# Optimization experiments

Hardware: AMD Instinct MI355X
Metric: run time of the kernel (lower is better)

Reference implementation:

```python
import jax, jax.numpy as jnp
import numpy as np

N_NODES = 100000
N_EDGES = 1600000
IN_DIM, HID_DIM, OUT_DIM = 64, 64, 16


def setup_inputs() -> dict:
    key = jax.random.key(0)
    k1, k2, k3, k4 = jax.random.split(key, 4)
    x = jax.random.normal(k1, (N_NODES, IN_DIM), dtype=jnp.float32)
    edge_index = jax.random.randint(k2, (2, N_EDGES), 0, N_NODES, dtype=jnp.int64)
    W1 = jax.random.normal(k3, (IN_DIM, HID_DIM), dtype=jnp.float32) * (1.0 / np.sqrt(IN_DIM))
    b1 = jnp.zeros((HID_DIM,), dtype=jnp.float32)
    W2 = jax.random.normal(k4, (HID_DIM, OUT_DIM), dtype=jnp.float32) * (1.0 / np.sqrt(HID_DIM))
    b2 = jnp.zeros((OUT_DIM,), dtype=jnp.float32)
    return {"x": x, "edge_index": edge_index, "W1": W1, "b1": b1, "W2": W2, "b2": b2}


def gcn_conv(x, src, dst, W, b, num_nodes):
    """GCNConv: h = D^{-1/2} (A+I) D^{-1/2} (x W) + b, edge-list form with self-loops already appended."""
    # symmetric degree normalization (degree counted at destination, incl. self-loops)
    deg = jax.ops.segment_sum(jnp.ones_like(dst, dtype=x.dtype), dst, num_segments=num_nodes)
    dinv = jnp.where(deg > 0, jax.lax.rsqrt(deg), 0.0)
    norm = dinv[src] * dinv[dst]                      # [E+N]
    h = x @ W                                         # [N, H] project first (fewer flops on edges)
    msg = h[src] * norm[:, None]                      # gather + scale, [E+N, H]
    out = jax.ops.segment_sum(msg, dst, num_segments=num_nodes)  # scatter-add
    return out + b


def reference(x, edge_index, W1, b1, W2, b2):
    num_nodes = x.shape[0]
    loop = jnp.arange(num_nodes, dtype=edge_index.dtype)
    src = jnp.concatenate([edge_index[0], loop])      # add self-loops once, reuse for both layers
    dst = jnp.concatenate([edge_index[1], loop])
    h = gcn_conv(x, src, dst, W1, b1, num_nodes)
    h = jax.nn.relu(h)
    # F.dropout(training=self.training): eval mode -> identity
    out = gcn_conv(h, src, dst, W2, b2, num_nodes)
    return out
```

## Files before the change

kernel.cpp:

```cpp
#include <hip/hip_runtime.h>

constexpr int N_NODES = 100000;
constexpr int F1 = 64;
constexpr int F2 = 16;
constexpr int SH = 7;
constexpr int NPB = 128;
constexpr int NBINS = (N_NODES + NPB - 1) / NPB;
constexpr int CAPB = 2560;
constexpr int TILE = 4096;
constexpr int GSTRIDE = 16;

static __device__ __forceinline__ unsigned short f2bf(float f) {
    unsigned int u = __float_as_uint(f);
    unsigned int r = (u + 0x7fffu + ((u >> 16) & 1u)) >> 16;
    return (unsigned short)r;
}
static __device__ __forceinline__ float bf2f(unsigned short b) {
    return __uint_as_float(((unsigned int)b) << 16);
}

__global__ __launch_bounds__(512) void k_bin(const int* __restrict__ src,
                                             const int* __restrict__ dst, int E,
                                             unsigned int* __restrict__ gcnt,
                                             unsigned int* __restrict__ entries) {
    __shared__ unsigned int cnt[NBINS];
    __shared__ unsigned int cur[NBINS];
    int tid = threadIdx.x;
    int base = blockIdx.x * TILE;
    int end = min(base + TILE, E);
    for (int i = tid; i < NBINS; i += 512) cnt[i] = 0;
    __syncthreads();
    for (int e = base + tid; e < end; e += 512) atomicAdd(&cnt[dst[e] >> SH], 1u);
    __syncthreads();
    for (int i = tid; i < NBINS; i += 512) {
        unsigned int c = cnt[i];
        cur[i] = (unsigned int)i * CAPB + (c ? atomicAdd(&gcnt[i * GSTRIDE], c) : 0u);
    }
    __syncthreads();
    for (int e = base + tid; e < end; e += 512) {
        int d = dst[e];
        int s = src[e];
        int bb = d >> SH;
        unsigned int p = atomicAdd(&cur[bb], 1u);
        if (p - (unsigned int)bb * CAPB < CAPB)
            entries[p] = (unsigned int)s | ((unsigned int)(d & (NPB - 1)) << 17);
    }
}

__global__ __launch_bounds__(512) void k_xw1(const float* __restrict__ x,
                                             const float* __restrict__ W,
                                             const unsigned int* __restrict__ gcnt,
                                             const unsigned int* __restrict__ entries,
                                             float* __restrict__ dinv,
                                             unsigned short* __restrict__ hs) {
    constexpr int XS = 68;
    __shared__ float Ws[64 * 64];
    __shared__ float xs[128 * XS];
    __shared__ unsigned int ncnt[NPB];
    __shared__ float dinvs[NPB];
    int tid = threadIdx.x;
    int b = blockIdx.x;
    int r0 = b * NPB;
    for (int i = tid; i < 1024; i += 512) {
        int k = i >> 4, c4 = (i & 15) << 2;
        *(float4*)&Ws[k * 64 + c4] = *(const float4*)&W[k * 64 + c4];
    }
    for (int i = tid; i < 2048; i += 512) {
        int rr = i >> 4, c4 = (i & 15) << 2;
        int r = r0 + rr;
        float4 v = make_float4(0.f, 0.f, 0.f, 0.f);
        if (r < N_NODES) v = *(const float4*)&x[(size_t)r * 64 + c4];
        *(float4*)&xs[rr * XS + c4] = v;
    }
    if (tid < NPB) ncnt[tid] = 0;
    __syncthreads();
    unsigned int cntE = gcnt[b * GSTRIDE]; if (cntE > CAPB) cntE = CAPB;
    unsigned int ebase = (unsigned int)b * CAPB;
    for (unsigned int e = tid; e < cntE; e += 512)
        atomicAdd(&ncnt[entries[ebase + e] >> 17], 1u);
    __syncthreads();
    if (tid < NPB) {
        int node = r0 + tid;
        float dv = rsqrtf((float)(ncnt[tid] + 1u));
        dinvs[tid] = dv;
        if (node < N_NODES) dinv[node] = dv;
    }
    __syncthreads();
    int tx = tid & 15, ty = tid >> 4;
    int c0 = tx << 2, rb = ty << 2;
    float acc[4][4] = {};
#pragma unroll 8
    for (int k = 0; k < 64; ++k) {
        float4 w = *(float4*)&Ws[k * 64 + c0];
        float x0 = xs[(rb + 0) * XS + k];
        float x1 = xs[(rb + 1) * XS + k];
        float x2 = xs[(rb + 2) * XS + k];
        float x3 = xs[(rb + 3) * XS + k];
        acc[0][0] += x0 * w.x; acc[0][1] += x0 * w.y; acc[0][2] += x0 * w.z; acc[0][3] += x0 * w.w;
        acc[1][0] += x1 * w.x; acc[1][1] += x1 * w.y; acc[1][2] += x1 * w.z; acc[1][3] += x1 * w.w;
        acc[2][0] += x2 * w.x; acc[2][1] += x2 * w.y; acc[2][2] += x2 * w.z; acc[2][3] += x2 * w.w;
        acc[3][0] += x3 * w.x; acc[3][1] += x3 * w.y; acc[3][2] += x3 * w.z; acc[3][3] += x3 * w.w;
    }
#pragma unroll
    for (int i = 0; i < 4; ++i) {
        int r = r0 + rb + i;
        if (r >= N_NODES) break;
        float dv = dinvs[rb + i];
        ushort4 p;
        p.x = f2bf(acc[i][0] * dv);
        p.y = f2bf(acc[i][1] * dv);
        p.z = f2bf(acc[i][2] * dv);
        p.w = f2bf(acc[i][3] * dv);
        *(ushort4*)&hs[(size_t)r * 64 + c0] = p;
    }
}

__global__ __launch_bounds__(1024) void k_agg1f(const unsigned int* __restrict__ gcnt,
                                                unsigned int* __restrict__ entries,
                                                unsigned int* __restrict__ noffg,
                                                const unsigned short* __restrict__ hs,
                                                const float* __restrict__ dinv,
                                                unsigned short* __restrict__ out1) {
    __shared__ unsigned int ncnt[NPB];
    __shared__ unsigned int noff[NPB + 1];
    __shared__ unsigned int cur[NPB];
    __shared__ unsigned int sl[CAPB];
    int tid = threadIdx.x;
    int b = blockIdx.x;
    unsigned int cntE = gcnt[b * GSTRIDE]; if (cntE > CAPB) cntE = CAPB;
    unsigned int base = (unsigned int)b * CAPB;
    if (tid < NPB) ncnt[tid] = 0;
    __syncthreads();
    for (unsigned int e = tid; e < cntE; e += 1024)
        atomicAdd(&ncnt[entries[base + e] >> 17], 1u);
    __syncthreads();
    if (tid < NPB) cur[tid] = ncnt[tid];
    __syncthreads();
    for (int ofs = 1; ofs < NPB; ofs <<= 1) {
        unsigned int v = (tid < NPB && tid >= ofs) ? cur[tid - ofs] : 0u;
        __syncthreads();
        if (tid < NPB) cur[tid] += v;
        __syncthreads();
    }
    if (tid < NPB) noff[tid + 1] = cur[tid];
    if (tid == 0) noff[0] = 0;
    __syncthreads();
    if (tid < NPB) cur[tid] = noff[tid];
    __syncthreads();
    for (unsigned int e = tid; e < cntE; e += 1024) {
        unsigned int v = entries[base + e];
        unsigned int p = atomicAdd(&cur[v >> 17], 1u);
        sl[p] = v & 0x1FFFFu;
    }
    __syncthreads();
    for (unsigned int e = tid; e < cntE; e += 1024) entries[base + e] = sl[e];
    if (tid <= NPB) noffg[b * (NPB + 1) + tid] = noff[tid];
    int wid = tid >> 6, k = tid & 63;
    for (int n = wid; n < NPB; n += 16) {
        int node = b * NPB + n;
        if (node >= N_NODES) break;
        unsigned int j = noff[n], jend = noff[n + 1];
        float acc = bf2f(hs[(size_t)node * 64 + k]);
        for (; j + 8 <= jend; j += 8) {
            unsigned int s0 = sl[j], s1 = sl[j + 1], s2 = sl[j + 2], s3 = sl[j + 3];
            unsigned int s4 = sl[j + 4], s5 = sl[j + 5], s6 = sl[j + 6], s7 = sl[j + 7];
            float a0 = bf2f(hs[(size_t)s0 * 64 + k]);
            float a1 = bf2f(hs[(size_t)s1 * 64 + k]);
            float a2 = bf2f(hs[(size_t)s2 * 64 + k]);
            float a3 = bf2f(hs[(size_t)s3 * 64 + k]);
            float a4 = bf2f(hs[(size_t)s4 * 64 + k]);
            float a5 = bf2f(hs[(size_t)s5 * 64 + k]);
            float a6 = bf2f(hs[(size_t)s6 * 64 + k]);
            float a7 = bf2f(hs[(size_t)s7 * 64 + k]);
            acc += ((a0 + a1) + (a2 + a3)) + ((a4 + a5) + (a6 + a7));
        }
        for (; j + 4 <= jend; j += 4) {
            unsigned int s0 = sl[j], s1 = sl[j + 1], s2 = sl[j + 2], s3 = sl[j + 3];
            float a0 = bf2f(hs[(size_t)s0 * 64 + k]);
            float a1 = bf2f(hs[(size_t)s1 * 64 + k]);
            float a2 = bf2f(hs[(size_t)s2 * 64 + k]);
            float a3 = bf2f(hs[(size_t)s3 * 64 + k]);
            acc += (a0 + a1) + (a2 + a3);
        }
        for (; j < jend; ++j) acc += bf2f(hs[(size_t)sl[j] * 64 + k]);
        out1[(size_t)node * 64 + k] = f2bf(acc * dinv[node]);
    }
}

__global__ __launch_bounds__(256) void k_xw2(const unsigned short* __restrict__ out1,
                                             const float* __restrict__ b1,
                                             const float* __restrict__ W2,
                                             const float* __restrict__ dinv,
                                             unsigned short* __restrict__ h2s) {
    constexpr int RS = 66;
    __shared__ float Ws[64 * 16];
    __shared__ float rs[128 * RS];
    __shared__ float b1s[64];
    int tid = threadIdx.x;
    int r0 = blockIdx.x * 128;
    if (tid < 64) b1s[tid] = b1[tid];
    for (int i = tid; i < 256; i += 256)
        *(float4*)&Ws[i * 4] = *(const float4*)&W2[i * 4];
    __syncthreads();
    for (int i = tid; i < 2048; i += 256) {
        int rr = i >> 4, c4 = (i & 15) << 2;
        int r = r0 + rr;
        float v0 = 0.f, v1 = 0.f, v2 = 0.f, v3 = 0.f;
        if (r < N_NODES) {
            ushort4 u = *(const ushort4*)&out1[(size_t)r * 64 + c4];
            v0 = fmaxf(bf2f(u.x) + b1s[c4 + 0], 0.f);
            v1 = fmaxf(bf2f(u.y) + b1s[c4 + 1], 0.f);
            v2 = fmaxf(bf2f(u.z) + b1s[c4 + 2], 0.f);
            v3 = fmaxf(bf2f(u.w) + b1s[c4 + 3], 0.f);
        }
        float* pp = &rs[rr * RS + c4];
        pp[0] = v0; pp[1] = v1; pp[2] = v2; pp[3] = v3;
    }
    __syncthreads();
    int tx = tid & 3, ty = tid >> 2;
    int c0 = tx << 2, rb = ty << 1;
    float acc[2][4] = {};
#pragma unroll 8
    for (int k = 0; k < 64; ++k) {
        float4 w = *(float4*)&Ws[k * 16 + c0];
        float x0 = rs[(rb + 0) * RS + k];
        float x1 = rs[(rb + 1) * RS + k];
        acc[0][0] += x0 * w.x; acc[0][1] += x0 * w.y; acc[0][2] += x0 * w.z; acc[0][3] += x0 * w.w;
        acc[1][0] += x1 * w.x; acc[1][1] += x1 * w.y; acc[1][2] += x1 * w.z; acc[1][3] += x1 * w.w;
    }
#pragma unroll
    for (int i = 0; i < 2; ++i) {
        int r = r0 + rb + i;
        if (r >= N_NODES) break;
        float dv = dinv[r];
        ushort4 p;
        p.x = f2bf(acc[i][0] * dv);
        p.y = f2bf(acc[i][1] * dv);
        p.z = f2bf(acc[i][2] * dv);
        p.w = f2bf(acc[i][3] * dv);
        *(ushort4*)&h2s[(size_t)r * 16 + c0] = p;
    }
}

__global__ __launch_bounds__(1024) void k_agg2f(const unsigned int* __restrict__ gcnt,
                                                const unsigned int* __restrict__ sorted,
                                                const unsigned int* __restrict__ noffg,
                                                const unsigned short* __restrict__ h2s,
                                                const float* __restrict__ dinv,
                                                const float* __restrict__ b2,
                                                float* __restrict__ out) {
    __shared__ unsigned int noff[NPB + 1];
    __shared__ unsigned int sl[CAPB];
    int tid = threadIdx.x;
    int b = blockIdx.x;
    unsigned int cntE = gcnt[b * GSTRIDE]; if (cntE > CAPB) cntE = CAPB;
    unsigned int base = (unsigned int)b * CAPB;
    if (tid <= NPB) noff[tid] = noffg[b * (NPB + 1) + tid];
    for (unsigned int e = tid; e < cntE; e += 1024) sl[e] = sorted[base + e];
    __syncthreads();
    int wid = tid >> 6, lane = tid & 63;
    int k = lane & 15, esub = lane >> 4;
    for (int n = wid; n < NPB; n += 16) {
        int node = b * NPB + n;
        if (node >= N_NODES) break;
        unsigned int j0 = noff[n], jend = noff[n + 1];
        float acc = 0.0f;
        unsigned int j = j0 + esub;
        for (; j + 4 < jend; j += 8) {
            float a = bf2f(h2s[(size_t)sl[j] * 16 + k]);
            float c = bf2f(h2s[(size_t)sl[j + 4] * 16 + k]);
            acc += a + c;
        }
        if (j < jend) acc += bf2f(h2s[(size_t)sl[j] * 16 + k]);
        acc += __shfl_xor(acc, 16);
        acc += __shfl_xor(acc, 32);
        if (lane < 16)
            out[(size_t)node * 16 + k] = (acc + bf2f(h2s[(size_t)node * 16 + k])) * dinv[node] + b2[k];
    }
}

static inline size_t align256(size_t x) { return (x + 255) & ~size_t(255); }

extern "C" void kernel_launch(void* const* d_in, const int* in_sizes, int n_in,
                              void* d_out, int out_size, void* d_ws, size_t ws_size,
                              hipStream_t stream) {
    const float* x  = (const float*)d_in[0];
    const int* edge = (const int*)d_in[1];
    const float* W1 = (const float*)d_in[2];
    const float* b1 = (const float*)d_in[3];
    const float* W2 = (const float*)d_in[4];
    const float* b2 = (const float*)d_in[5];
    float* out = (float*)d_out;

    const int E = in_sizes[1] / 2;
    const int* src = edge;
    const int* dst = edge + E;

    char* ws = (char*)d_ws;
    size_t o = 0;
    unsigned int* gcnt    = (unsigned int*)(ws + o); o += align256((size_t)NBINS * GSTRIDE * 4);
    float* dinv           = (float*)(ws + o);        o += align256((size_t)N_NODES * 4);
    unsigned int* entries = (unsigned int*)(ws + o); o += align256((size_t)NBINS * CAPB * 4);
    unsigned int* noffg   = (unsigned int*)(ws + o); o += align256((size_t)NBINS * (NPB + 1) * 4);
    unsigned short* hs    = (unsigned short*)(ws + o); o += align256((size_t)N_NODES * F1 * 2);
    unsigned short* out1  = (unsigned short*)(ws + o); o += align256((size_t)N_NODES * F1 * 2);
    unsigned short* h2s   = (unsigned short*)(ws + o); o += align256((size_t)N_NODES * F2 * 2);

    hipMemsetAsync(gcnt, 0, (size_t)NBINS * GSTRIDE * 4, stream);

    k_bin<<<(E + TILE - 1) / TILE, 512, 0, stream>>>(src, dst, E, gcnt, entries);

    k_xw1<<<NBINS, 512, 0, stream>>>(x, W1, gcnt, entries, dinv, hs);
    k_agg1f<<<NBINS, 1024, 0, stream>>>(gcnt, entries, noffg, hs, dinv, out1);

    k_xw2<<<(N_NODES + 127) / 128, 256, 0, stream>>>(out1, b1, W2, dinv, h2s);
    k_agg2f<<<NBINS, 1024, 0, stream>>>(gcnt, entries, noffg, h2s, dinv, b2, out);
}
```

Baseline: 144.4 us.

## Split layer-1 aggregation across two blocks per bin by feature half

```diff
diff --git a/kernel.cpp b/kernel.cpp
--- a/kernel.cpp
+++ b/kernel.cpp
@@ -116,7 +116,8 @@
 }
 
 __global__ __launch_bounds__(1024) void k_agg1f(const unsigned int* __restrict__ gcnt,
-                                                unsigned int* __restrict__ entries,
+                                                const unsigned int* __restrict__ entries,
+                                                unsigned int* __restrict__ sorted,
                                                 unsigned int* __restrict__ noffg,
                                                 const unsigned short* __restrict__ hs,
                                                 const float* __restrict__ dinv,
@@ -126,7 +127,10 @@
     __shared__ unsigned int cur[NPB];
     __shared__ unsigned int sl[CAPB];
     int tid = threadIdx.x;
-    int b = blockIdx.x;
+    int blk = blockIdx.x;
+    int half = (blk & 7) >= 4;
+    int b = ((blk >> 3) << 2) + (blk & 3);
+    if (b >= NBINS) return;
     unsigned int cntE = gcnt[b * GSTRIDE]; if (cntE > CAPB) cntE = CAPB;
     unsigned int base = (unsigned int)b * CAPB;
     if (tid < NPB) ncnt[tid] = 0;
@@ -153,37 +157,30 @@
         sl[p] = v & 0x1FFFFu;
     }
     __syncthreads();
-    for (unsigned int e = tid; e < cntE; e += 1024) entries[base + e] = sl[e];
-    if (tid <= NPB) noffg[b * (NPB + 1) + tid] = noff[tid];
-    int wid = tid >> 6, k = tid & 63;
+    if (half == 0) {
+        for (unsigned int e = tid; e < cntE; e += 1024) sorted[base + e] = sl[e];
+        if (tid <= NPB) noffg[b * (NPB + 1) + tid] = noff[tid];
+    }
+    int wid = tid >> 6, lane = tid & 63;
+    int grp = lane >> 5;
+    int c = half * 32 + (lane & 31);
     for (int n = wid; n < NPB; n += 16) {
         int node = b * NPB + n;
         if (node >= N_NODES) break;
-        unsigned int j = noff[n], jend = noff[n + 1];
-        float acc = bf2f(hs[(size_t)node * 64 + k]);
-        for (; j + 8 <= jend; j += 8) {
-            unsigned int s0 = sl[j], s1 = sl[j + 1], s2 = sl[j + 2], s3 = sl[j + 3];
-            unsigned int s4 = sl[j + 4], s5 = sl[j + 5], s6 = sl[j + 6], s7 = sl[j + 7];
-            float a0 = bf2f(hs[(size_t)s0 * 64 + k]);
-            float a1 = bf2f(hs[(size_t)s1 * 64 + k]);
-            float a2 = bf2f(hs[(size_t)s2 * 64 + k]);
-            float a3 = bf2f(hs[(size_t)s3 * 64 + k]);
-            float a4 = bf2f(hs[(size_t)s4 * 64 + k]);
-            float a5 = bf2f(hs[(size_t)s5 * 64 + k]);
-            float a6 = bf2f(hs[(size_t)s6 * 64 + k]);
-            float a7 = bf2f(hs[(size_t)s7 * 64 + k]);
-            acc += ((a0 + a1) + (a2 + a3)) + ((a4 + a5) + (a6 + a7));
-        }
-        for (; j + 4 <= jend; j += 4) {
-            unsigned int s0 = sl[j], s1 = sl[j + 1], s2 = sl[j + 2], s3 = sl[j + 3];
-            float a0 = bf2f(hs[(size_t)s0 * 64 + k]);
-            float a1 = bf2f(hs[(size_t)s1 * 64 + k]);
-            float a2 = bf2f(hs[(size_t)s2 * 64 + k]);
-            float a3 = bf2f(hs[(size_t)s3 * 64 + k]);
+        unsigned int j = noff[n] + (unsigned)grp, jend = noff[n + 1];
+        float acc = grp ? 0.f : bf2f(hs[(size_t)node * 64 + c]);
+        for (; j + 6 < jend; j += 8) {
+            unsigned int s0 = sl[j], s1 = sl[j + 2], s2 = sl[j + 4], s3 = sl[j + 6];
+            float a0 = bf2f(hs[(size_t)s0 * 64 + c]);
+            float a1 = bf2f(hs[(size_t)s1 * 64 + c]);
+            float a2 = bf2f(hs[(size_t)s2 * 64 + c]);
+            float a3 = bf2f(hs[(size_t)s3 * 64 + c]);
             acc += (a0 + a1) + (a2 + a3);
         }
-        for (; j < jend; ++j) acc += bf2f(hs[(size_t)sl[j] * 64 + k]);
-        out1[(size_t)node * 64 + k] = f2bf(acc * dinv[node]);
+        for (; j < jend; j += 2) acc += bf2f(hs[(size_t)sl[j] * 64 + c]);
+        acc += __shfl_xor(acc, 32);
+        if (lane < 32)
+            out1[(size_t)node * 64 + c] = f2bf(acc * dinv[node]);
     }
 }
 
@@ -301,6 +298,7 @@
     unsigned int* gcnt    = (unsigned int*)(ws + o); o += align256((size_t)NBINS * GSTRIDE * 4);
     float* dinv           = (float*)(ws + o);        o += align256((size_t)N_NODES * 4);
     unsigned int* entries = (unsigned int*)(ws + o); o += align256((size_t)NBINS * CAPB * 4);
+    unsigned int* sorted  = (unsigned int*)(ws + o); o += align256((size_t)NBINS * CAPB * 4);
     unsigned int* noffg   = (unsigned int*)(ws + o); o += align256((size_t)NBINS * (NPB + 1) * 4);
     unsigned short* hs    = (unsigned short*)(ws + o); o += align256((size_t)N_NODES * F1 * 2);
     unsigned short* out1  = (unsigned short*)(ws + o); o += align256((size_t)N_NODES * F1 * 2);
@@ -311,8 +309,11 @@
     k_bin<<<(E + TILE - 1) / TILE, 512, 0, stream>>>(src, dst, E, gcnt, entries);
 
     k_xw1<<<NBINS, 512, 0, stream>>>(x, W1, gcnt, entries, dinv, hs);
-    k_agg1f<<<NBINS, 1024, 0, stream>>>(gcnt, entries, noffg, hs, dinv, out1);
+    {
+        int halfblocks = ((2 * NBINS + 7) / 8) * 8;
+        k_agg1f<<<halfblocks, 1024, 0, stream>>>(gcnt, entries, sorted, noffg, hs, dinv, out1);
+    }
 
     k_xw2<<<(N_NODES + 127) / 128, 256, 0, stream>>>(out1, b1, W2, dinv, h2s);
-    k_agg2f<<<NBINS, 1024, 0, stream>>>(gcnt, entries, noffg, h2s, dinv, b2, out);
-}
+    k_agg2f<<<NBINS, 1024, 0, stream>>>(gcnt, sorted, noffg, h2s, dinv, b2, out);
+}
```

After: 181.6 us. +25.8%, slower.

## Stage binned edges in LDS and write them out coalesced via block prefix scan

Applied to the files above, without the earlier changes.

```diff
diff --git a/kernel.cpp b/kernel.cpp
--- a/kernel.cpp
+++ b/kernel.cpp
@@ -7,7 +7,7 @@
 constexpr int NPB = 128;
 constexpr int NBINS = (N_NODES + NPB - 1) / NPB;
 constexpr int CAPB = 2560;
-constexpr int TILE = 4096;
+constexpr int TILE = 8192;
 constexpr int GSTRIDE = 16;
 
 static __device__ __forceinline__ unsigned short f2bf(float f) {
@@ -19,31 +19,60 @@
     return __uint_as_float(((unsigned int)b) << 16);
 }
 
-__global__ __launch_bounds__(512) void k_bin(const int* __restrict__ src,
-                                             const int* __restrict__ dst, int E,
-                                             unsigned int* __restrict__ gcnt,
-                                             unsigned int* __restrict__ entries) {
+__global__ __launch_bounds__(1024) void k_bin(const int* __restrict__ src,
+                                              const int* __restrict__ dst, int E,
+                                              unsigned int* __restrict__ gcnt,
+                                              unsigned int* __restrict__ entries) {
     __shared__ unsigned int cnt[NBINS];
-    __shared__ unsigned int cur[NBINS];
+    __shared__ unsigned int gbase[NBINS];
+    __shared__ unsigned int ebuf[TILE];
+    __shared__ unsigned short pbin[TILE];
     int tid = threadIdx.x;
     int base = blockIdx.x * TILE;
     int end = min(base + TILE, E);
-    for (int i = tid; i < NBINS; i += 512) cnt[i] = 0;
-    __syncthreads();
-    for (int e = base + tid; e < end; e += 512) atomicAdd(&cnt[dst[e] >> SH], 1u);
-    __syncthreads();
-    for (int i = tid; i < NBINS; i += 512) {
-        unsigned int c = cnt[i];
-        cur[i] = (unsigned int)i * CAPB + (c ? atomicAdd(&gcnt[i * GSTRIDE], c) : 0u);
-    }
-    __syncthreads();
-    for (int e = base + tid; e < end; e += 512) {
-        int d = dst[e];
-        int s = src[e];
-        int bb = d >> SH;
-        unsigned int p = atomicAdd(&cur[bb], 1u);
-        if (p - (unsigned int)bb * CAPB < CAPB)
-            entries[p] = (unsigned int)s | ((unsigned int)(d & (NPB - 1)) << 17);
+    int tcount = end - base;
+    int e0 = base + tid * 8;
+    int nle = e0 < end ? min(8, end - e0) : 0;
+    int ds[8], ss[8];
+#pragma unroll
+    for (int i = 0; i < 8; ++i) {
+        if (i < nle) { ds[i] = dst[e0 + i]; ss[i] = src[e0 + i]; }
+    }
+    for (int i = tid; i < NBINS; i += 1024) cnt[i] = 0;
+    __syncthreads();
+#pragma unroll
+    for (int i = 0; i < 8; ++i)
+        if (i < nle) atomicAdd(&cnt[ds[i] >> SH], 1u);
+    __syncthreads();
+    unsigned int ccount = (tid < NBINS) ? cnt[tid] : 0u;
+    for (int ofs = 1; ofs < 1024; ofs <<= 1) {
+        unsigned int v = (tid < NBINS && tid >= ofs) ? cnt[tid - ofs] : 0u;
+        __syncthreads();
+        if (tid < NBINS) cnt[tid] += v;
+        __syncthreads();
+    }
+    if (tid < NBINS) {
+        unsigned int excl = cnt[tid] - ccount;
+        unsigned int alloc = ccount ? atomicAdd(&gcnt[tid * GSTRIDE], ccount) : 0u;
+        gbase[tid] = (unsigned int)tid * CAPB + alloc - excl;
+        cnt[tid] = excl;
+    }
+    __syncthreads();
+#pragma unroll
+    for (int i = 0; i < 8; ++i) {
+        if (i < nle) {
+            int d = ds[i];
+            int b = d >> SH;
+            unsigned int p = atomicAdd(&cnt[b], 1u);
+            ebuf[p] = (unsigned int)ss[i] | ((unsigned int)(d & (NPB - 1)) << 17);
+            pbin[p] = (unsigned short)b;
+        }
+    }
+    __syncthreads();
+    for (int p = tid; p < tcount; p += 1024) {
+        unsigned int b = pbin[p];
+        unsigned int gpos = gbase[b] + (unsigned int)p;
+        if (gpos - b * CAPB < CAPB) entries[gpos] = ebuf[p];
     }
 }
 
@@ -308,7 +337,7 @@
 
     hipMemsetAsync(gcnt, 0, (size_t)NBINS * GSTRIDE * 4, stream);
 
-    k_bin<<<(E + TILE - 1) / TILE, 512, 0, stream>>>(src, dst, E, gcnt, entries);
+    k_bin<<<(E + TILE - 1) / TILE, 1024, 0, stream>>>(src, dst, E, gcnt, entries);
 
     k_xw1<<<NBINS, 512, 0, stream>>>(x, W1, gcnt, entries, dinv, hs);
     k_agg1f<<<NBINS, 1024, 0, stream>>>(gcnt, entries, noffg, hs, dinv, out1);
```

Result: faster. 136.8 us (median of 2 runs) (-5.2%).
